# Performance work log

Measured on AMD Instinct MI355X. Metric: run time of the kernel, lower is better.

Reference implementation:

```python
import jax, jax.numpy as jnp
import numpy as np

N_NODES = 100000
N_EDGES = 1600000
N_RELS = 4
F_IN, H_DIM, OUT_DIM = 128, 64, 64
N_LAYERS = 3  # num_hidden_layers=2 h2h layers + 1 h2o layer (all 64->64 here)


def setup_inputs() -> dict:
    key = jax.random.key(0)
    ks = jax.random.split(key, 10)
    h = jax.random.normal(ks[0], (N_NODES, F_IN), dtype=jnp.float32)
    src = jax.random.randint(ks[1], (N_EDGES,), 0, N_NODES, dtype=jnp.int32)
    dst = jax.random.randint(ks[2], (N_EDGES,), 0, N_NODES, dtype=jnp.int32)
    etypes = jax.random.randint(ks[3], (N_EDGES,), 0, N_RELS, dtype=jnp.int32)
    # parameters, scaled ~1/sqrt(fan_in) for numerical sanity through ReLU stack
    W_fc = jax.random.normal(ks[4], (F_IN, H_DIM), dtype=jnp.float32) / np.sqrt(F_IN)
    W_rels = jax.random.normal(ks[5], (N_LAYERS, N_RELS, H_DIM, H_DIM), dtype=jnp.float32) / np.sqrt(H_DIM)
    W_loops = jax.random.normal(ks[6], (N_LAYERS, H_DIM, H_DIM), dtype=jnp.float32) / np.sqrt(H_DIM)
    biases = jnp.zeros((N_LAYERS, H_DIM), dtype=jnp.float32)
    W_dense = jax.random.normal(ks[7], (OUT_DIM, 1), dtype=jnp.float32) / np.sqrt(OUT_DIM)
    b_dense = jnp.zeros((1,), dtype=jnp.float32)
    return {"h": h, "src": src, "dst": dst, "etypes": etypes,
            "W_fc": W_fc, "W_rels": W_rels, "W_loops": W_loops,
            "biases": biases, "W_dense": W_dense, "b_dense": b_dense}


def reference(h, src, dst, etypes, W_fc, W_rels, W_loops, biases, W_dense, b_dense):
    n = h.shape[0]
    # GATLayer.forward returns g.ndata['z'] (fc projection); the attention
    # aggregate written to 'h' by reduce_func is never read in the original.
    x = h @ W_fc  # (N, H)
    # RelGraphConv stack: msg = W_{r(e)} h_src, sum over in-edges, + self-loop + bias, ReLU
    for l in range(N_LAYERS):
        # transform every node under every relation, then gather per edge
        xw = jnp.einsum('nd,rde->rne', x, W_rels[l])        # (R, N, H)
        msg = xw[etypes, src]                                # (E, H)
        agg = jax.ops.segment_sum(msg, dst, num_segments=n)  # (N, H)
        x = jax.nn.relu(agg + x @ W_loops[l] + biases[l])
    # SumPooling over the single graph; h viewed as (N, 1, OUT_DIM)
    pooled = jnp.sum(x.reshape(n, -1, OUT_DIM), axis=0)[None]  # (1, 1, OUT_DIM)
    out = pooled @ W_dense + b_dense                            # (1, 1, 1)
    return out
```

## Files before the change

kernel.cpp:

```cpp
#include <hip/hip_runtime.h>



__global__ void k_degree(const int* __restrict__ dst, int* __restrict__ deg, int E) {
  int i = blockIdx.x * blockDim.x + threadIdx.x;
  if (i < E) atomicAdd(&deg[dst[i]], 1);
}

__global__ __launch_bounds__(1024) void k_scan1(const int* __restrict__ deg,
                                                int* __restrict__ scan,
                                                int* __restrict__ part, int N) {
  __shared__ int s[1024];
  int tid = threadIdx.x;
  int idx = blockIdx.x * 1024 + tid;
  int v = (idx < N) ? deg[idx] : 0;
  s[tid] = v;
  __syncthreads();
  for (int off = 1; off < 1024; off <<= 1) {
    int t = (tid >= off) ? s[tid - off] : 0;
    __syncthreads();
    s[tid] += t;
    __syncthreads();
  }
  if (idx < N) scan[idx] = s[tid];
  if (tid == 1023) part[blockIdx.x] = s[1023];
}

__global__ __launch_bounds__(1024) void k_scan2(const int* __restrict__ part,
                                                int* __restrict__ partx, int nblk) {
  __shared__ int s[1024];
  int tid = threadIdx.x;
  int v = (tid < nblk) ? part[tid] : 0;
  s[tid] = v;
  __syncthreads();
  for (int off = 1; off < 1024; off <<= 1) {
    int t = (tid >= off) ? s[tid - off] : 0;
    __syncthreads();
    s[tid] += t;
    __syncthreads();
  }
  if (tid < nblk) partx[tid] = s[tid] - v;
}

__global__ void k_scan3(const int* __restrict__ scan, const int* __restrict__ deg,
                        const int* __restrict__ partx, int* __restrict__ rowptr,
                        int* __restrict__ cursor, int N, int E) {
  int i = blockIdx.x * blockDim.x + threadIdx.x;
  if (i < N) {
    int v = scan[i] - deg[i] + partx[i >> 10];
    rowptr[i] = v;
    cursor[i] = v;
  }
  if (i == 0) rowptr[N] = E;
}

__global__ void k_scatter(const int* __restrict__ src, const int* __restrict__ dst,
                          const int* __restrict__ et, int* __restrict__ cursor,
                          unsigned* __restrict__ edata, int E) {
  int i = blockIdx.x * blockDim.x + threadIdx.x;
  if (i < E) {
    int d = dst[i];
    int pos = atomicAdd(&cursor[d], 1);
    edata[pos] = (unsigned)src[i] | ((unsigned)et[i] << 17);
  }
}


__global__ __launch_bounds__(256) void k_agg(const int* __restrict__ rowptr,
                                             const unsigned* __restrict__ edata,
                                             const float* __restrict__ x,
                                             float* __restrict__ pre, int N) {
  int wid = (blockIdx.x * blockDim.x + threadIdx.x) >> 6;
  int lane = threadIdx.x & 63;
  if (wid >= N) return;
  int beg = rowptr[wid];
  int end = rowptr[wid + 1];
  float a0 = 0.f, a1 = 0.f, a2 = 0.f, a3 = 0.f;
  int e = beg;
  for (; e + 4 <= end; e += 4) {
    unsigned p0 = __builtin_amdgcn_readfirstlane(edata[e]);
    unsigned p1 = __builtin_amdgcn_readfirstlane(edata[e + 1]);
    unsigned p2 = __builtin_amdgcn_readfirstlane(edata[e + 2]);
    unsigned p3 = __builtin_amdgcn_readfirstlane(edata[e + 3]);
    float v0 = x[(size_t)(p0 & 0x1FFFF) * 64 + lane];
    float v1 = x[(size_t)(p1 & 0x1FFFF) * 64 + lane];
    float v2 = x[(size_t)(p2 & 0x1FFFF) * 64 + lane];
    float v3 = x[(size_t)(p3 & 0x1FFFF) * 64 + lane];
    { int t = p0 >> 17; if (t == 0) a0 += v0; else if (t == 1) a1 += v0; else if (t == 2) a2 += v0; else a3 += v0; }
    { int t = p1 >> 17; if (t == 0) a0 += v1; else if (t == 1) a1 += v1; else if (t == 2) a2 += v1; else a3 += v1; }
    { int t = p2 >> 17; if (t == 0) a0 += v2; else if (t == 1) a1 += v2; else if (t == 2) a2 += v2; else a3 += v2; }
    { int t = p3 >> 17; if (t == 0) a0 += v3; else if (t == 1) a1 += v3; else if (t == 2) a2 += v3; else a3 += v3; }
  }
  for (; e < end; ++e) {
    unsigned p = __builtin_amdgcn_readfirstlane(edata[e]);
    float v = x[(size_t)(p & 0x1FFFF) * 64 + lane];
    int t = p >> 17;
    if (t == 0) a0 += v; else if (t == 1) a1 += v; else if (t == 2) a2 += v; else a3 += v;
  }
  float* o = pre + (size_t)wid * 256 + lane;
  o[0] = a0; o[64] = a1; o[128] = a2; o[192] = a3;
}


__global__ __launch_bounds__(256) void k_gemm(
    const float* __restrict__ A0, int K0,
    const float* __restrict__ A1, int K1,
    const float* __restrict__ B0, const float* __restrict__ B1,
    const float* __restrict__ bias, int relu,
    float* __restrict__ C, int M) {
  __shared__ float As[32][132];
  __shared__ float Bs[32][64];
  const int tid = threadIdx.x;
  const int tx = tid & 15;
  const int ty = tid >> 4;
  const int row0 = blockIdx.x * 128;

  float acc[8][4];
#pragma unroll
  for (int i = 0; i < 8; ++i)
#pragma unroll
    for (int j = 0; j < 4; ++j) acc[i][j] = 0.f;

  const int K = K0 + K1;
  for (int kb = 0; kb < K; kb += 32) {
    const float* Ap; int lda, kloc;
    const float* Bp;
    if (kb < K0) { Ap = A0; lda = K0; kloc = kb;      Bp = B0 + kb * 64; }
    else         { Ap = A1; lda = K1; kloc = kb - K0; Bp = B1 + (kb - K0) * 64; }

    {
      const int r = tid >> 1;
      const int kk0 = (tid & 1) * 16;
      const int grow = row0 + r;
      float vv[16];
      if (grow < M) {
        const float* s = Ap + (size_t)grow * lda + kloc + kk0;
#pragma unroll
        for (int q = 0; q < 4; ++q)
          *reinterpret_cast<float4*>(&vv[q * 4]) =
              *reinterpret_cast<const float4*>(s + q * 4);
      } else {
#pragma unroll
        for (int q = 0; q < 16; ++q) vv[q] = 0.f;
      }
#pragma unroll
      for (int q = 0; q < 16; ++q) As[kk0 + q][r] = vv[q];
    }
    {
      const int kr = tid >> 3;
      const int f0 = (tid & 7) * 8;
      const float* s = Bp + kr * 64 + f0;
      *reinterpret_cast<float4*>(&Bs[kr][f0]) = *reinterpret_cast<const float4*>(s);
      *reinterpret_cast<float4*>(&Bs[kr][f0 + 4]) = *reinterpret_cast<const float4*>(s + 4);
    }
    __syncthreads();

#pragma unroll
    for (int kk = 0; kk < 32; ++kk) {
      float a[8], b[4];
      *reinterpret_cast<float4*>(&a[0]) = *reinterpret_cast<const float4*>(&As[kk][ty * 8]);
      *reinterpret_cast<float4*>(&a[4]) = *reinterpret_cast<const float4*>(&As[kk][ty * 8 + 4]);
      *reinterpret_cast<float4*>(&b[0]) = *reinterpret_cast<const float4*>(&Bs[kk][tx * 4]);
#pragma unroll
      for (int i = 0; i < 8; ++i)
#pragma unroll
        for (int j = 0; j < 4; ++j) acc[i][j] += a[i] * b[j];
    }
    __syncthreads();
  }

  float bc[4];
#pragma unroll
  for (int j = 0; j < 4; ++j) bc[j] = bias ? bias[tx * 4 + j] : 0.f;
#pragma unroll
  for (int i = 0; i < 8; ++i) {
    const int r = row0 + ty * 8 + i;
    if (r < M) {
      float o[4];
#pragma unroll
      for (int j = 0; j < 4; ++j) {
        float v = acc[i][j] + bc[j];
        o[j] = relu ? fmaxf(v, 0.f) : v;
      }
      *reinterpret_cast<float4*>(C + (size_t)r * 64 + tx * 4) =
          *reinterpret_cast<const float4*>(o);
    }
  }
}


__global__ __launch_bounds__(256) void k_pool(const float* __restrict__ x,
                                              const float* __restrict__ Wd,
                                              float* __restrict__ accum, int total) {
  __shared__ float red[256];
  int tid = threadIdx.x;
  float s = 0.f;
  for (int i = blockIdx.x * 256 + tid; i < total; i += gridDim.x * 256)
    s += x[i] * Wd[i & 63];
  red[tid] = s;
  __syncthreads();
  for (int off = 128; off > 0; off >>= 1) {
    if (tid < off) red[tid] += red[tid + off];
    __syncthreads();
  }
  if (tid == 0) atomicAdd(accum, red[0]);
}

__global__ void k_final(const float* __restrict__ accum, const float* __restrict__ b,
                        float* __restrict__ out) {
  out[0] = accum[0] + b[0];
}


extern "C" void kernel_launch(void* const* d_in, const int* in_sizes, int n_in,
                              void* d_out, int out_size, void* d_ws, size_t ws_size,
                              hipStream_t stream) {
  const float* h       = (const float*)d_in[0];
  const int*   src     = (const int*)d_in[1];
  const int*   dst     = (const int*)d_in[2];
  const int*   et      = (const int*)d_in[3];
  const float* W_fc    = (const float*)d_in[4];
  const float* W_rels  = (const float*)d_in[5];
  const float* W_loops = (const float*)d_in[6];
  const float* biases  = (const float*)d_in[7];
  const float* W_dense = (const float*)d_in[8];
  const float* b_dense = (const float*)d_in[9];
  float* out = (float*)d_out;

  const int N = in_sizes[0] / 128;
  const int E = in_sizes[1];

  size_t cur = 0;
  auto carve = [&](size_t bytes) -> char* {
    cur = (cur + 255) & ~(size_t)255;
    char* p = (char*)d_ws + cur;
    cur += bytes;
    return p;
  };
  int* deg        = (int*)carve((size_t)N * 4);
  int* scan       = (int*)carve((size_t)N * 4);
  int* part       = (int*)carve(1024 * 4);
  int* partx      = (int*)carve(1024 * 4);
  int* rowptr     = (int*)carve((size_t)(N + 1) * 4);
  int* cursor     = (int*)carve((size_t)N * 4);
  unsigned* edata = (unsigned*)carve((size_t)E * 4);
  float* xA       = (float*)carve((size_t)N * 64 * 4);
  float* xB       = (float*)carve((size_t)N * 64 * 4);
  float* pre      = (float*)carve((size_t)N * 256 * 4);
  float* accum    = (float*)carve(256);

  hipMemsetAsync(deg, 0, (size_t)N * 4, stream);
  hipMemsetAsync(accum, 0, 4, stream);

  const int eb = (E + 255) / 256;
  k_degree<<<eb, 256, 0, stream>>>(dst, deg, E);
  const int nblk = (N + 1023) / 1024;
  k_scan1<<<nblk, 1024, 0, stream>>>(deg, scan, part, N);
  k_scan2<<<1, 1024, 0, stream>>>(part, partx, nblk);
  k_scan3<<<(N + 255) / 256, 256, 0, stream>>>(scan, deg, partx, rowptr, cursor, N, E);
  k_scatter<<<eb, 256, 0, stream>>>(src, dst, et, cursor, edata, E);

  const int gb = (N + 127) / 128;
  k_gemm<<<gb, 256, 0, stream>>>(h, 128, nullptr, 0, W_fc, nullptr, nullptr, 0, xA, N);

  float* xin = xA;
  float* xout = xB;
  for (int l = 0; l < 3; ++l) {
    k_agg<<<(N + 3) / 4, 256, 0, stream>>>(rowptr, edata, xin, pre, N);
    k_gemm<<<gb, 256, 0, stream>>>(pre, 256, xin, 64,
                                   W_rels + (size_t)l * 4 * 64 * 64,
                                   W_loops + (size_t)l * 64 * 64,
                                   biases + (size_t)l * 64, 1, xout, N);
    float* t = xin; xin = xout; xout = t;
  }

  k_pool<<<1024, 256, 0, stream>>>(xin, W_dense, accum, N * 64);
  k_final<<<1, 1, 0, stream>>>(accum, b_dense, out);
}
```

Baseline: 751.1 us.

## Use split-bf16 MFMA GEMM and fuse sum pooling into final layer

Replaces the FP32 FMA-based GEMM with an MFMA bf16 kernel that splits each FP32 operand into three bf16 parts (hi/mid/lo) and accumulates six cross-products to emulate FP32 accuracy. Weights are pre-split and pre-swizzled once per call into MFMA lane layout by a small conversion kernel. The last layer's GEMM now performs the dense-weighted pooling reduction in its epilogue, skipping the final activation write and the separate pool kernel. In exchange it costs extra conversion ALU work on A tiles and six MFMAs per product, and it slightly changes rounding.

```diff
diff --git a/kernel.cpp b/kernel.cpp
--- a/kernel.cpp
+++ b/kernel.cpp
@@ -1,5 +1,18 @@
 #include <hip/hip_runtime.h>
 
+
+typedef __attribute__((ext_vector_type(8))) short short8;
+typedef __attribute__((ext_vector_type(4))) float f32x4;
+
+__device__ inline unsigned short f32_to_bf16_rne(float x) {
+  unsigned u = __builtin_bit_cast(unsigned, x);
+  unsigned r = (u + 0x7FFFu + ((u >> 16) & 1u)) >> 16;
+  return (unsigned short)r;
+}
+__device__ inline float bf16_bits_to_f32(unsigned short b) {
+  unsigned u = ((unsigned)b) << 16;
+  return __builtin_bit_cast(float, u);
+}
 
 
 __global__ void k_degree(const int* __restrict__ dst, int* __restrict__ deg, int E) {
@@ -102,108 +115,158 @@
 }
 
 
-__global__ __launch_bounds__(256) void k_gemm(
+__global__ void k_bconv(const float* __restrict__ B0, int K0,
+                        const float* __restrict__ B1, int K1,
+                        unsigned short* __restrict__ Bh,
+                        unsigned short* __restrict__ Bm,
+                        unsigned short* __restrict__ Bl) {
+  int K = K0 + K1;
+  int idx = blockIdx.x * 256 + threadIdx.x;
+  if (idx >= K * 64) return;
+  int k = idx >> 6, col = idx & 63;
+  float v;
+  if (k < K0)      v = B0[(size_t)k * 64 + col];
+  else if (k < K)  v = B1[(size_t)(k - K0) * 64 + col];
+  else             v = 0.f;
+  int kstep = k >> 5, kk = k & 31;
+  int ct = col >> 4;
+  int lane = (col & 15) + (((kk >> 3)) << 4);
+  int j = kk & 7;
+  size_t o = (((size_t)(kstep * 4 + ct)) * 64 + lane) * 8 + j;
+  unsigned short hb = f32_to_bf16_rne(v);
+  float r1 = v - bf16_bits_to_f32(hb);
+  unsigned short mb = f32_to_bf16_rne(r1);
+  unsigned short lb = f32_to_bf16_rne(r1 - bf16_bits_to_f32(mb));
+  Bh[o] = hb; Bm[o] = mb; Bl[o] = lb;
+}
+
+
+__global__ __launch_bounds__(256) void k_mgemm(
     const float* __restrict__ A0, int K0,
     const float* __restrict__ A1, int K1,
-    const float* __restrict__ B0, const float* __restrict__ B1,
+    const unsigned short* __restrict__ Bh,
+    const unsigned short* __restrict__ Bm,
+    const unsigned short* __restrict__ Bl,
     const float* __restrict__ bias, int relu,
-    float* __restrict__ C, int M) {
-  __shared__ float As[32][132];
-  __shared__ float Bs[32][64];
+    float* __restrict__ C, int M,
+    const float* __restrict__ Wd, float* __restrict__ accum, int pool) {
+  __shared__ short8 Ah[8 * 64], Am[8 * 64], Al[8 * 64];
+  __shared__ float red[256];
+
   const int tid = threadIdx.x;
-  const int tx = tid & 15;
-  const int ty = tid >> 4;
+  const int wave = tid >> 6;
+  const int lane = tid & 63;
   const int row0 = blockIdx.x * 128;
-
-  float acc[8][4];
-#pragma unroll
-  for (int i = 0; i < 8; ++i)
-#pragma unroll
-    for (int j = 0; j < 4; ++j) acc[i][j] = 0.f;
-
   const int K = K0 + K1;
+
+  f32x4 acc[2][4];
+#pragma unroll
+  for (int i = 0; i < 2; ++i)
+#pragma unroll
+    for (int j = 0; j < 4; ++j) acc[i][j] = (f32x4){0.f, 0.f, 0.f, 0.f};
+
+  const int srow = tid >> 1;
+  const int kk0 = (tid & 1) * 16;
+  const int rt_s = srow >> 4;
+  const int laneA = (srow & 15) + ((kk0 >> 3) << 4);
+
   for (int kb = 0; kb < K; kb += 32) {
-    const float* Ap; int lda, kloc;
-    const float* Bp;
-    if (kb < K0) { Ap = A0; lda = K0; kloc = kb;      Bp = B0 + kb * 64; }
-    else         { Ap = A1; lda = K1; kloc = kb - K0; Bp = B1 + (kb - K0) * 64; }
-
     {
-      const int r = tid >> 1;
-      const int kk0 = (tid & 1) * 16;
-      const int grow = row0 + r;
-      float vv[16];
+      const float* Ap;
+      int lda;
+      if (kb < K0) { Ap = A0 + kb; lda = K0; }
+      else         { Ap = A1 + (kb - K0); lda = K1; }
+      const int grow = row0 + srow;
+      float v[16];
       if (grow < M) {
-        const float* s = Ap + (size_t)grow * lda + kloc + kk0;
+        const float* s = Ap + (size_t)grow * lda + kk0;
 #pragma unroll
         for (int q = 0; q < 4; ++q)
-          *reinterpret_cast<float4*>(&vv[q * 4]) =
+          *reinterpret_cast<float4*>(&v[q * 4]) =
               *reinterpret_cast<const float4*>(s + q * 4);
       } else {
 #pragma unroll
-        for (int q = 0; q < 16; ++q) vv[q] = 0.f;
+        for (int q = 0; q < 16; ++q) v[q] = 0.f;
       }
-#pragma unroll
-      for (int q = 0; q < 16; ++q) As[kk0 + q][r] = vv[q];
+      short h[16], m[16], l[16];
+#pragma unroll
+      for (int q = 0; q < 16; ++q) {
+        unsigned short hb = f32_to_bf16_rne(v[q]);
+        float r1 = v[q] - bf16_bits_to_f32(hb);
+        unsigned short mb = f32_to_bf16_rne(r1);
+        unsigned short lb = f32_to_bf16_rne(r1 - bf16_bits_to_f32(mb));
+        h[q] = (short)hb; m[q] = (short)mb; l[q] = (short)lb;
+      }
+      short8 H0 = {h[0], h[1], h[2], h[3], h[4], h[5], h[6], h[7]};
+      short8 H1 = {h[8], h[9], h[10], h[11], h[12], h[13], h[14], h[15]};
+      short8 M0 = {m[0], m[1], m[2], m[3], m[4], m[5], m[6], m[7]};
+      short8 M1 = {m[8], m[9], m[10], m[11], m[12], m[13], m[14], m[15]};
+      short8 L0 = {l[0], l[1], l[2], l[3], l[4], l[5], l[6], l[7]};
+      short8 L1 = {l[8], l[9], l[10], l[11], l[12], l[13], l[14], l[15]};
+      Ah[rt_s * 64 + laneA] = H0;
+      Ah[rt_s * 64 + laneA + 16] = H1;
+      Am[rt_s * 64 + laneA] = M0;
+      Am[rt_s * 64 + laneA + 16] = M1;
+      Al[rt_s * 64 + laneA] = L0;
+      Al[rt_s * 64 + laneA + 16] = L1;
     }
-    {
-      const int kr = tid >> 3;
-      const int f0 = (tid & 7) * 8;
-      const float* s = Bp + kr * 64 + f0;
-      *reinterpret_cast<float4*>(&Bs[kr][f0]) = *reinterpret_cast<const float4*>(s);
-      *reinterpret_cast<float4*>(&Bs[kr][f0 + 4]) = *reinterpret_cast<const float4*>(s + 4);
+    __syncthreads();
+
+    const int rt0 = wave * 2, rt1 = rt0 + 1;
+    short8 ah0 = Ah[rt0 * 64 + lane], ah1 = Ah[rt1 * 64 + lane];
+    short8 am0 = Am[rt0 * 64 + lane], am1 = Am[rt1 * 64 + lane];
+    short8 al0 = Al[rt0 * 64 + lane], al1 = Al[rt1 * 64 + lane];
+    const int kstep = kb >> 5;
+#pragma unroll
+    for (int ct = 0; ct < 4; ++ct) {
+      size_t bo = (((size_t)(kstep * 4 + ct)) * 64 + lane) * 8;
+      short8 bh = *reinterpret_cast<const short8*>(&Bh[bo]);
+      short8 bm = *reinterpret_cast<const short8*>(&Bm[bo]);
+      short8 bl = *reinterpret_cast<const short8*>(&Bl[bo]);
+      acc[0][ct] = __builtin_amdgcn_mfma_f32_16x16x32_bf16(ah0, bh, acc[0][ct], 0, 0, 0);
+      acc[0][ct] = __builtin_amdgcn_mfma_f32_16x16x32_bf16(ah0, bm, acc[0][ct], 0, 0, 0);
+      acc[0][ct] = __builtin_amdgcn_mfma_f32_16x16x32_bf16(am0, bh, acc[0][ct], 0, 0, 0);
+      acc[0][ct] = __builtin_amdgcn_mfma_f32_16x16x32_bf16(ah0, bl, acc[0][ct], 0, 0, 0);
+      acc[0][ct] = __builtin_amdgcn_mfma_f32_16x16x32_bf16(al0, bh, acc[0][ct], 0, 0, 0);
+      acc[0][ct] = __builtin_amdgcn_mfma_f32_16x16x32_bf16(am0, bm, acc[0][ct], 0, 0, 0);
+      acc[1][ct] = __builtin_amdgcn_mfma_f32_16x16x32_bf16(ah1, bh, acc[1][ct], 0, 0, 0);
+      acc[1][ct] = __builtin_amdgcn_mfma_f32_16x16x32_bf16(ah1, bm, acc[1][ct], 0, 0, 0);
+      acc[1][ct] = __builtin_amdgcn_mfma_f32_16x16x32_bf16(am1, bh, acc[1][ct], 0, 0, 0);
+      acc[1][ct] = __builtin_amdgcn_mfma_f32_16x16x32_bf16(ah1, bl, acc[1][ct], 0, 0, 0);
+      acc[1][ct] = __builtin_amdgcn_mfma_f32_16x16x32_bf16(al1, bh, acc[1][ct], 0, 0, 0);
+      acc[1][ct] = __builtin_amdgcn_mfma_f32_16x16x32_bf16(am1, bm, acc[1][ct], 0, 0, 0);
     }
     __syncthreads();
-
-#pragma unroll
-    for (int kk = 0; kk < 32; ++kk) {
-      float a[8], b[4];
-      *reinterpret_cast<float4*>(&a[0]) = *reinterpret_cast<const float4*>(&As[kk][ty * 8]);
-      *reinterpret_cast<float4*>(&a[4]) = *reinterpret_cast<const float4*>(&As[kk][ty * 8 + 4]);
-      *reinterpret_cast<float4*>(&b[0]) = *reinterpret_cast<const float4*>(&Bs[kk][tx * 4]);
-#pragma unroll
-      for (int i = 0; i < 8; ++i)
-#pragma unroll
-        for (int j = 0; j < 4; ++j) acc[i][j] += a[i] * b[j];
+  }
+
+  float local = 0.f;
+#pragma unroll
+  for (int rt = 0; rt < 2; ++rt) {
+#pragma unroll
+    for (int ct = 0; ct < 4; ++ct) {
+      const int col = ct * 16 + (lane & 15);
+      const float bc = bias ? bias[col] : 0.f;
+#pragma unroll
+      for (int reg = 0; reg < 4; ++reg) {
+        const int grow = row0 + wave * 32 + rt * 16 + (lane >> 4) * 4 + reg;
+        if (grow < M) {
+          float y = acc[rt][ct][reg] + bc;
+          if (relu) y = fmaxf(y, 0.f);
+          if (pool) local += y * Wd[col];
+          else C[(size_t)grow * 64 + col] = y;
+        }
+      }
     }
-    __syncthreads();
-  }
-
-  float bc[4];
-#pragma unroll
-  for (int j = 0; j < 4; ++j) bc[j] = bias ? bias[tx * 4 + j] : 0.f;
-#pragma unroll
-  for (int i = 0; i < 8; ++i) {
-    const int r = row0 + ty * 8 + i;
-    if (r < M) {
-      float o[4];
-#pragma unroll
-      for (int j = 0; j < 4; ++j) {
-        float v = acc[i][j] + bc[j];
-        o[j] = relu ? fmaxf(v, 0.f) : v;
-      }
-      *reinterpret_cast<float4*>(C + (size_t)r * 64 + tx * 4) =
-          *reinterpret_cast<const float4*>(o);
+  }
+  if (pool) {
+    red[tid] = local;
+    __syncthreads();
+    for (int off = 128; off > 0; off >>= 1) {
+      if (tid < off) red[tid] += red[tid + off];
+      __syncthreads();
     }
-  }
-}
-
-
-__global__ __launch_bounds__(256) void k_pool(const float* __restrict__ x,
-                                              const float* __restrict__ Wd,
-                                              float* __restrict__ accum, int total) {
-  __shared__ float red[256];
-  int tid = threadIdx.x;
-  float s = 0.f;
-  for (int i = blockIdx.x * 256 + tid; i < total; i += gridDim.x * 256)
-    s += x[i] * Wd[i & 63];
-  red[tid] = s;
-  __syncthreads();
-  for (int off = 128; off > 0; off >>= 1) {
-    if (tid < off) red[tid] += red[tid + off];
-    __syncthreads();
-  }
-  if (tid == 0) atomicAdd(accum, red[0]);
+    if (tid == 0) atomicAdd(accum, red[0]);
+  }
 }
 
 __global__ void k_final(const float* __restrict__ accum, const float* __restrict__ b,
@@ -248,9 +311,21 @@
   float* xB       = (float*)carve((size_t)N * 64 * 4);
   float* pre      = (float*)carve((size_t)N * 256 * 4);
   float* accum    = (float*)carve(256);
+  unsigned short* Bfc[3];
+  for (int p = 0; p < 3; ++p) Bfc[p] = (unsigned short*)carve((size_t)128 * 64 * 2);
+  unsigned short* Blay[3][3];
+  for (int l = 0; l < 3; ++l)
+    for (int p = 0; p < 3; ++p) Blay[l][p] = (unsigned short*)carve((size_t)320 * 64 * 2);
 
   hipMemsetAsync(deg, 0, (size_t)N * 4, stream);
   hipMemsetAsync(accum, 0, 4, stream);
+
+  k_bconv<<<(128 * 64 + 255) / 256, 256, 0, stream>>>(W_fc, 128, nullptr, 0,
+                                                      Bfc[0], Bfc[1], Bfc[2]);
+  for (int l = 0; l < 3; ++l)
+    k_bconv<<<(320 * 64 + 255) / 256, 256, 0, stream>>>(
+        W_rels + (size_t)l * 4 * 64 * 64, 256, W_loops + (size_t)l * 64 * 64, 64,
+        Blay[l][0], Blay[l][1], Blay[l][2]);
 
   const int eb = (E + 255) / 256;
   k_degree<<<eb, 256, 0, stream>>>(dst, deg, E);
@@ -261,19 +336,22 @@
   k_scatter<<<eb, 256, 0, stream>>>(src, dst, et, cursor, edata, E);
 
   const int gb = (N + 127) / 128;
-  k_gemm<<<gb, 256, 0, stream>>>(h, 128, nullptr, 0, W_fc, nullptr, nullptr, 0, xA, N);
+  k_mgemm<<<gb, 256, 0, stream>>>(h, 128, nullptr, 0,
+                                  Bfc[0], Bfc[1], Bfc[2],
+                                  nullptr, 0, xA, N, nullptr, nullptr, 0);
 
   float* xin = xA;
   float* xout = xB;
   for (int l = 0; l < 3; ++l) {
     k_agg<<<(N + 3) / 4, 256, 0, stream>>>(rowptr, edata, xin, pre, N);
-    k_gemm<<<gb, 256, 0, stream>>>(pre, 256, xin, 64,
-                                   W_rels + (size_t)l * 4 * 64 * 64,
-                                   W_loops + (size_t)l * 64 * 64,
-                                   biases + (size_t)l * 64, 1, xout, N);
+    const int last = (l == 2);
+    k_mgemm<<<gb, 256, 0, stream>>>(pre, 256, xin, 64,
+                                    Blay[l][0], Blay[l][1], Blay[l][2],
+                                    biases + (size_t)l * 64, 1,
+                                    last ? nullptr : xout, N,
+                                    last ? W_dense : nullptr, accum, last);
     float* t = xin; xin = xout; xout = t;
   }
 
-  k_pool<<<1024, 256, 0, stream>>>(xin, W_dense, accum, N * 64);
   k_final<<<1, 1, 0, stream>>>(accum, b_dense, out);
 }
```

Result: faster. 667.6 us (-11.1%).
